# Kernel optimization log

Measured on AMD Instinct MI355X. Metric: run time of the kernel, lower is better.

Reference implementation:

```python
import jax, jax.numpy as jnp
import numpy as np

B, W, L = 32768, 5, 20            # batch, words per example, max chars per word
WV, CV = 50000, 100               # word vocab, char vocab
CE, OC, K = 32, 30, 3             # char embed dim, conv out channels (=window_size), kernel
WE, HID, TAGS = 50, 100, 36       # word embed dim, fc1 hidden, output tags


def setup_inputs() -> dict:
    key = jax.random.key(0)
    ks = jax.random.split(key, 8)
    inp = jax.random.randint(ks[0], (B, W, 1 + L), 0, 100, dtype=jnp.int32)
    embedding_matrix = jax.random.normal(ks[1], (WV, WE), jnp.float32).at[0].set(0.0)  # padding_idx=0, frozen
    char_emb = jax.random.normal(ks[2], (CV, CE), jnp.float32).at[0].set(0.0)          # padding_idx=0
    conv_w = jax.random.normal(ks[3], (OC, CE, K), jnp.float32) * 0.1
    conv_b = jnp.zeros((OC,), jnp.float32)
    fc1_w = jax.random.normal(ks[4], (HID, (WE + OC) * W), jnp.float32) * 0.05
    fc1_b = jnp.zeros((HID,), jnp.float32)
    out_w = jax.random.normal(ks[5], (TAGS, HID), jnp.float32) * 0.1
    out_b = jnp.zeros((TAGS,), jnp.float32)
    return dict(input=inp, embedding_matrix=embedding_matrix, char_emb=char_emb,
                conv_w=conv_w, conv_b=conv_b, fc1_w=fc1_w, fc1_b=fc1_b,
                out_w=out_w, out_b=out_b)


def reference(input, embedding_matrix, char_emb, conv_w, conv_b, fc1_w, fc1_b, out_w, out_b):
    b = input.shape[0]
    word_ids = input[:, :, 0]                 # [B, W]
    char_ids = input[:, :, 1:]                # [B, W, L]
    we = embedding_matrix[word_ids]           # [B, W, 50]
    ce = char_emb[char_ids]                   # [B, W, L, CE]
    # conv1d over char axis, batched over all B*W words at once
    x = ce.reshape(b * W, L, CE).transpose(0, 2, 1)        # [B*W, CE, L]
    conv = jax.lax.conv_general_dilated(
        x, conv_w, window_strides=(1,), padding='VALID',
        dimension_numbers=('NCH', 'OIH', 'NCH')) + conv_b[None, :, None]  # [B*W, OC, L-2]
    pooled = conv.max(axis=2).reshape(b, W, OC)            # max pool over time
    feats = jnp.concatenate([we, pooled], axis=-1).reshape(b, -1)  # [B, (50+OC)*W]
    h = jnp.tanh(feats @ fc1_w.T + fc1_b)     # dropout is a no-op at inference
    return h @ out_w.T + out_b                # [B, 36]
```

## Files before the change

kernel.cpp:

```cpp
#include <hip/hip_runtime.h>

#define B_TOT 32768
#define OC 30
#define HID 100
#define TAGS 36

#define WS_TH  0
#define WS_FC1 6000
#define WS_OUT 32624

typedef __attribute__((ext_vector_type(8))) _Float16 half8;
typedef __attribute__((ext_vector_type(2))) _Float16 h2v;
typedef __attribute__((ext_vector_type(4))) float f32x4;

__device__ inline half8 ash8(uint4 u) {
    union { uint4 a; half8 b; } v; v.a = u; return v.b;
}
__device__ inline unsigned int h2u(h2v h) {
    union { h2v a; unsigned int b; } v; v.a = h; return v.b;
}
__device__ inline h2v u2h(unsigned int u) {
    union { unsigned int a; h2v b; } v; v.a = u; return v.b;
}
__device__ inline unsigned int pk_f16(float a, float b) {
    h2v h; h.x = (_Float16)a; h.y = (_Float16)b; return h2u(h);
}
__device__ inline float fast_tanh(float x) {
    float ax = __builtin_fabsf(x);
    float e  = __expf(2.0f * ax);
    float r  = 1.0f - 2.0f * __builtin_amdgcn_rcpf(e + 1.0f);
    return __builtin_copysignf(r, x);
}

__global__ void prep(const float* __restrict__ conv_w,
                     const float* __restrict__ char_emb,
                     const float* __restrict__ fc1_w,
                     const float* __restrict__ out_w,
                     unsigned int* __restrict__ ws) {
    int idx = blockIdx.x * 256 + threadIdx.x;
    if (idx < 6000) {
        int d  = idx & 3;
        int t  = idx >> 2;
        int c  = t % 100;
        int kg = t / 100;
        int g  = kg % 5, k = kg / 5;
        int rd = g * 4 + d;
        float v[2];
        #pragma unroll
        for (int e = 0; e < 2; ++e) {
            int oc = rd * 2 + e;
            float s = 0.f;
            if (oc < OC) {
                for (int ce = 0; ce < 32; ++ce)
                    s += char_emb[c * 32 + ce] * conv_w[(oc * 32 + ce) * 3 + k];
            }
            v[e] = s;
        }
        ws[WS_TH + idx] = pk_f16(v[0], v[1]);
    } else if (idx < 6000 + 23296) {
        int t = idx - 6000;
        int dw = t & 3, lane = (t >> 2) & 63, chunk = t >> 8;
        int ks = chunk / 7, nt = chunk % 7;
        int j = nt * 16 + (lane & 15);
        int k = ks * 32 + (lane >> 4) * 8 + dw * 2;
        float a = (j < HID && k     < 400) ? fc1_w[j * 400 + k]     : 0.f;
        float b = (j < HID && k + 1 < 400) ? fc1_w[j * 400 + k + 1] : 0.f;
        ws[WS_FC1 + ks * 2048 + (nt * 64 + lane) * 4 + dw] = pk_f16(a, b);
    } else if (idx < 29296 + 3072) {
        int t = idx - 29296;
        int dw = t & 3, lane = (t >> 2) & 63, chunk = t >> 8;
        int ks = chunk / 3, nt = chunk % 3;
        int j = nt * 16 + (lane & 15);
        int k = ks * 32 + (lane >> 4) * 8 + dw * 2;
        float a = (j < TAGS && k     < HID) ? out_w[j * 100 + k]     : 0.f;
        float b = (j < TAGS && k + 1 < HID) ? out_w[j * 100 + k + 1] : 0.f;
        ws[WS_OUT + t] = pk_f16(a, b);
    }
}

__global__ __launch_bounds__(256, 2)
void fused(const int*   __restrict__ input,
           const float* __restrict__ emb,
           const float* __restrict__ conv_b,
           const float* __restrict__ fc1_b,
           const float* __restrict__ out_b,
           const unsigned int* __restrict__ ws,
           float*       __restrict__ out)
{
    __shared__ __align__(16) unsigned int Ths[6000];
    __shared__ __align__(16) unsigned int FL[64 * 212];

    const int tid  = threadIdx.x;
    const int wv   = tid >> 6;
    const int lane = tid & 63;
    const int ln15 = lane & 15;
    const int quad = lane >> 4;
    const int gi0  = blockIdx.x * 64 + wv * 16;
    unsigned int* Fw = &FL[wv * (16 * 212)];

    const uint4* srcB = (const uint4*)(ws + WS_FC1);
    const int se = wv * 128 + lane;

    {
        const uint4* src = (const uint4*)(ws + WS_TH);
        uint4* dst = (uint4*)Ths;
        for (int idx = tid; idx < 1500; idx += 256) dst[idx] = src[idx];
    }
    uint4 p0 = srcB[se], p1 = srcB[se + 64];
    __syncthreads();

    #pragma unroll
    for (int r = 0; r < 2; ++r) {
        int idx = lane + r * 64;
        Fw[(idx >> 3) * 212 + 200 + (idx & 7)] = 0;
    }

    #pragma unroll 4
    for (int idx = lane; idx < 2000; idx += 64) {
        int ph = idx % 25;
        int w  = (idx / 25) % 5;
        int i  = idx / 125;
        int wid = input[(gi0 + i) * 105 + w * 21];
        float2 e = *(const float2*)&emb[wid * 50 + ph * 2];
        Fw[i * 212 + w * 40 + ph] = pk_f16(e.x, e.y);
    }

    {
        const int q4  = lane & 3;
        const int oc0 = q4 * 8;
        h2v bias[4];
        #pragma unroll
        for (int d = 0; d < 4; ++d) {
            int a = oc0 + 2 * d, b = a + 1;
            bias[d].x = (_Float16)(a < OC ? conv_b[a] : 0.f);
            bias[d].y = (_Float16)(b < OC ? conv_b[b] : 0.f);
        }
        const unsigned int* T0 = &Ths[q4 * 400];
        const unsigned int* T1 = &Ths[q4 * 400 + 2000];
        const unsigned int* T2 = &Ths[q4 * 400 + 4000];
        #pragma unroll
        for (int it = 0; it < 5; ++it) {
            int task = (lane >> 2) + it * 16;
            int i = task / 5, w = task % 5;
            const int* cp = &input[(gi0 + i) * 105 + w * 21 + 1];
            int c[20];
            #pragma unroll
            for (int p = 0; p < 20; ++p) c[p] = cp[p];
            h2v m[4];
            #pragma unroll
            for (int d = 0; d < 4; ++d) { m[d].x = (_Float16)(-30000.f); m[d].y = (_Float16)(-30000.f); }
            #pragma unroll 6
            for (int p = 0; p < 18; ++p) {
                uint4 ra = *(const uint4*)&T0[c[p    ] * 4];
                uint4 rb = *(const uint4*)&T1[c[p + 1] * 4];
                uint4 rc = *(const uint4*)&T2[c[p + 2] * 4];
                unsigned int* pa = (unsigned int*)&ra;
                unsigned int* pb = (unsigned int*)&rb;
                unsigned int* pc = (unsigned int*)&rc;
                #pragma unroll
                for (int d = 0; d < 4; ++d) {
                    h2v s = u2h(pa[d]) + u2h(pb[d]) + u2h(pc[d]);
                    m[d] = __builtin_elementwise_max(m[d], s);
                }
            }
            int base = i * 212 + w * 40 + 25 + q4 * 4;
            Fw[base]     = h2u(m[0] + bias[0]);
            Fw[base + 1] = h2u(m[1] + bias[1]);
            Fw[base + 2] = h2u(m[2] + bias[2]);
            if (q4 < 3) Fw[base + 3] = h2u(m[3] + bias[3]);
        }
    }

    uint4 af[13];
    {
        const unsigned int* arow = &Fw[ln15 * 212 + quad * 4];
        #pragma unroll
        for (int ks = 0; ks < 13; ++ks) af[ks] = *(const uint4*)(arow + ks * 16);
    }

    f32x4 acc[7];
    #pragma unroll
    for (int t = 0; t < 7; ++t) acc[t] = f32x4{0, 0, 0, 0};

    uint4* Bb = (uint4*)Ths;
    __syncthreads();
    Bb[se] = p0; Bb[se + 64] = p1;
    __syncthreads();

    #pragma unroll
    for (int ks = 0; ks < 13; ++ks) {
        uint4 n0, n1;
        if (ks < 12) {
            n0 = srcB[(ks + 1) * 512 + se];
            n1 = srcB[(ks + 1) * 512 + se + 64];
        }
        const uint4* bp = Bb + (ks & 1) * 512;
        half8 a = ash8(af[ks]);
        #pragma unroll
        for (int t = 0; t < 7; ++t)
            acc[t] = __builtin_amdgcn_mfma_f32_16x16x32_f16(a, ash8(bp[t * 64 + lane]), acc[t], 0, 0, 0);
        if (ks < 12) {
            uint4* np = Bb + ((ks + 1) & 1) * 512;
            np[se] = n0; np[se + 64] = n1;
        }
        __syncthreads();
    }

    const uint4* srcO = (const uint4*)(ws + WS_OUT);
    uint4 o0 = srcO[wv * 192 + lane];
    uint4 o1 = srcO[wv * 192 + 64 + lane];
    uint4 o2 = srcO[wv * 192 + 128 + lane];

    unsigned int* Hw = Fw;
    {
        for (int t2 = lane; t2 < 224; t2 += 64) {
            int i = t2 / 14, d = t2 % 14;
            Hw[i * 68 + 50 + d] = 0;
        }
        unsigned short* Hs = (unsigned short*)Hw;
        #pragma unroll
        for (int t = 0; t < 7; ++t) {
            int j = t * 16 + ln15;
            if (j < HID) {
                float bj = fc1_b[j];
                #pragma unroll
                for (int r = 0; r < 4; ++r) {
                    int it = quad * 4 + r;
                    float hv = fast_tanh(acc[t][r] + bj);
                    _Float16 h = (_Float16)hv;
                    Hs[it * 136 + j] = *reinterpret_cast<unsigned short*>(&h);
                }
            }
        }
    }

    Bb[wv * 192 + lane]       = o0;
    Bb[wv * 192 + 64 + lane]  = o1;
    Bb[wv * 192 + 128 + lane] = o2;
    __syncthreads();

    {
        f32x4 oacc[3];
        #pragma unroll
        for (int t = 0; t < 3; ++t) oacc[t] = f32x4{0, 0, 0, 0};
        const int aoff = ln15 * 68 + quad * 4;
        #pragma unroll
        for (int ks = 0; ks < 4; ++ks) {
            half8 a = ash8(*(const uint4*)&Hw[aoff + ks * 16]);
            #pragma unroll
            for (int t = 0; t < 3; ++t) {
                uint4 bv = Bb[(ks * 3 + t) * 64 + lane];
                oacc[t] = __builtin_amdgcn_mfma_f32_16x16x32_f16(a, ash8(bv), oacc[t], 0, 0, 0);
            }
        }
        #pragma unroll
        for (int t = 0; t < 3; ++t) {
            int o = t * 16 + ln15;
            if (o < TAGS) {
                float bo = out_b[o];
                #pragma unroll
                for (int r = 0; r < 4; ++r) {
                    int it = gi0 + quad * 4 + r;
                    out[it * TAGS + o] = oacc[t][r] + bo;
                }
            }
        }
    }
}

extern "C" void kernel_launch(void* const* d_in, const int* in_sizes, int n_in,
                              void* d_out, int out_size, void* d_ws, size_t ws_size,
                              hipStream_t stream) {
    const int*   input  = (const int*)  d_in[0];
    const float* emb    = (const float*)d_in[1];
    const float* char_e = (const float*)d_in[2];
    const float* conv_w = (const float*)d_in[3];
    const float* conv_b = (const float*)d_in[4];
    const float* fc1_w  = (const float*)d_in[5];
    const float* fc1_b  = (const float*)d_in[6];
    const float* out_w  = (const float*)d_in[7];
    const float* out_b  = (const float*)d_in[8];
    unsigned int* ws = (unsigned int*)d_ws;

    prep<<<127, 256, 0, stream>>>(conv_w, char_e, fc1_w, out_w, ws);
    fused<<<B_TOT / 64, 256, 0, stream>>>(input, emb, conv_b, fc1_b, out_b, ws, (float*)d_out);
}
```

Baseline: 111.1 us.

## Triple-buffer fc1 weight staging and pad conv table rows against bank conflicts

The fc1 B-operand staging goes from a double buffer of 512 uint4 per k-step to a triple buffer of 448 uint4. Only the 7 real n-tiles are copied, with all 256 threads sharing the copy, and the global prefetch runs two steps ahead. One barrier is removed from the last iteration. The conv lookup table is re-laid out with each 400-word slice padded to 404 words, to spread LDS bank accesses across the four q4 groups, and the workspace offsets are realigned to match. This adds register pressure from holding extra prefetched vectors and makes the index math more fragile.

Measured after the change: 113.7 us. 1.02x slower.

```diff
diff --git a/kernel.cpp b/kernel.cpp
--- a/kernel.cpp
+++ b/kernel.cpp
@@ -6,8 +6,8 @@
 #define TAGS 36
 
 #define WS_TH  0
-#define WS_FC1 6000
-#define WS_OUT 32624
+#define WS_FC1 6144
+#define WS_OUT 32768
 
 typedef __attribute__((ext_vector_type(8))) _Float16 half8;
 typedef __attribute__((ext_vector_type(2))) _Float16 h2v;
@@ -43,8 +43,9 @@
         int t  = idx >> 2;
         int c  = t % 100;
         int kg = t / 100;
-        int g  = kg % 5, k = kg / 5;
+        int g  = kg % 5;
         int rd = g * 4 + d;
+        int k  = kg / 5;
         float v[2];
         #pragma unroll
         for (int e = 0; e < 2; ++e) {
@@ -56,7 +57,7 @@
             }
             v[e] = s;
         }
-        ws[WS_TH + idx] = pk_f16(v[0], v[1]);
+        ws[WS_TH + kg * 404 + c * 4 + d] = pk_f16(v[0], v[1]);
     } else if (idx < 6000 + 23296) {
         int t = idx - 6000;
         int dw = t & 3, lane = (t >> 2) & 63, chunk = t >> 8;
@@ -87,7 +88,7 @@
            const unsigned int* __restrict__ ws,
            float*       __restrict__ out)
 {
-    __shared__ __align__(16) unsigned int Ths[6000];
+    __shared__ __align__(16) unsigned int Ths[6060];
     __shared__ __align__(16) unsigned int FL[64 * 212];
 
     const int tid  = threadIdx.x;
@@ -96,17 +97,20 @@
     const int ln15 = lane & 15;
     const int quad = lane >> 4;
     const int gi0  = blockIdx.x * 64 + wv * 16;
+    const bool lo192 = (tid < 192);
     unsigned int* Fw = &FL[wv * (16 * 212)];
 
     const uint4* srcB = (const uint4*)(ws + WS_FC1);
-    const int se = wv * 128 + lane;
 
     {
         const uint4* src = (const uint4*)(ws + WS_TH);
         uint4* dst = (uint4*)Ths;
-        for (int idx = tid; idx < 1500; idx += 256) dst[idx] = src[idx];
-    }
-    uint4 p0 = srcB[se], p1 = srcB[se + 64];
+        for (int idx = tid; idx < 1515; idx += 256) dst[idx] = src[idx];
+    }
+    uint4 z4 = {0, 0, 0, 0};
+    uint4 pA0 = srcB[tid],        pA1 = lo192 ? srcB[256 + tid]        : z4;
+    uint4 pB0 = srcB[512 + tid],  pB1 = lo192 ? srcB[512 + 256 + tid]  : z4;
+    uint4 pC0 = srcB[1024 + tid], pC1 = lo192 ? srcB[1024 + 256 + tid] : z4;
     __syncthreads();
 
     #pragma unroll
@@ -135,9 +139,9 @@
             bias[d].x = (_Float16)(a < OC ? conv_b[a] : 0.f);
             bias[d].y = (_Float16)(b < OC ? conv_b[b] : 0.f);
         }
-        const unsigned int* T0 = &Ths[q4 * 400];
-        const unsigned int* T1 = &Ths[q4 * 400 + 2000];
-        const unsigned int* T2 = &Ths[q4 * 400 + 4000];
+        const unsigned int* T0 = &Ths[q4 * 404];
+        const unsigned int* T1 = &Ths[q4 * 404 + 2020];
+        const unsigned int* T2 = &Ths[q4 * 404 + 4040];
         #pragma unroll
         for (int it = 0; it < 5; ++it) {
             int task = (lane >> 2) + it * 16;
@@ -184,26 +188,30 @@
 
     uint4* Bb = (uint4*)Ths;
     __syncthreads();
-    Bb[se] = p0; Bb[se + 64] = p1;
-    __syncthreads();
+    Bb[tid] = pA0;            if (lo192) Bb[256 + tid] = pA1;
+    Bb[448 + tid] = pB0;      if (lo192) Bb[448 + 256 + tid] = pB1;
+    __syncthreads();
+    uint4 f0 = pC0, f1 = pC1;
 
     #pragma unroll
     for (int ks = 0; ks < 13; ++ks) {
-        uint4 n0, n1;
-        if (ks < 12) {
-            n0 = srcB[(ks + 1) * 512 + se];
-            n1 = srcB[(ks + 1) * 512 + se + 64];
-        }
-        const uint4* bp = Bb + (ks & 1) * 512;
+        uint4 n0 = z4, n1 = z4;
+        if (ks <= 9) {
+            n0 = srcB[(ks + 3) * 512 + tid];
+            if (lo192) n1 = srcB[(ks + 3) * 512 + 256 + tid];
+        }
+        const uint4* bp = Bb + (ks % 3) * 448;
         half8 a = ash8(af[ks]);
         #pragma unroll
         for (int t = 0; t < 7; ++t)
             acc[t] = __builtin_amdgcn_mfma_f32_16x16x32_f16(a, ash8(bp[t * 64 + lane]), acc[t], 0, 0, 0);
-        if (ks < 12) {
-            uint4* np = Bb + ((ks + 1) & 1) * 512;
-            np[se] = n0; np[se + 64] = n1;
-        }
-        __syncthreads();
+        if (ks <= 10) {
+            uint4* np = Bb + ((ks + 2) % 3) * 448;
+            np[tid] = f0;
+            if (lo192) np[256 + tid] = f1;
+        }
+        f0 = n0; f1 = n1;
+        if (ks <= 10 || ks == 12) __syncthreads();
     }
 
     const uint4* srcO = (const uint4*)(ws + WS_OUT);
```

## Precompute pairwise char-bigram conv table to replace two lookups per tap

Applied to the files above, without the earlier changes.

The first two conv taps are folded into a 100x100 bigram table computed in the prep kernel and read from global memory, leaving only the third tap in LDS. Each position now needs two gathers and one add instead of three gathers and two adds, and LDS use drops. The cost is a much larger prep kernel (160k extra threads, each doing a 32-element dot product) and random 640 KB global/L2 gathers in the main loop in place of cheap LDS reads.

New measurement: 132.6 us. 19.4% more time.

```diff
diff --git a/kernel.cpp b/kernel.cpp
--- a/kernel.cpp
+++ b/kernel.cpp
@@ -6,8 +6,9 @@
 #define TAGS 36
 
 #define WS_TH  0
-#define WS_FC1 6000
-#define WS_OUT 32624
+#define WS_TB  2048
+#define WS_FC1 162048
+#define WS_OUT 188672
 
 typedef __attribute__((ext_vector_type(8))) _Float16 half8;
 typedef __attribute__((ext_vector_type(2))) _Float16 h2v;
@@ -38,27 +39,41 @@
                      const float* __restrict__ out_w,
                      unsigned int* __restrict__ ws) {
     int idx = blockIdx.x * 256 + threadIdx.x;
-    if (idx < 6000) {
-        int d  = idx & 3;
-        int t  = idx >> 2;
-        int c  = t % 100;
-        int kg = t / 100;
-        int g  = kg % 5, k = kg / 5;
-        int rd = g * 4 + d;
+    if (idx < 1600) {
+        int d = idx & 15, c = idx >> 4;
         float v[2];
         #pragma unroll
         for (int e = 0; e < 2; ++e) {
-            int oc = rd * 2 + e;
+            int oc = 2 * d + e;
             float s = 0.f;
             if (oc < OC) {
                 for (int ce = 0; ce < 32; ++ce)
-                    s += char_emb[c * 32 + ce] * conv_w[(oc * 32 + ce) * 3 + k];
+                    s += char_emb[c * 32 + ce] * conv_w[(oc * 32 + ce) * 3 + 2];
             }
             v[e] = s;
         }
-        ws[WS_TH + idx] = pk_f16(v[0], v[1]);
-    } else if (idx < 6000 + 23296) {
-        int t = idx - 6000;
+        ws[WS_TH + c * 20 + d] = pk_f16(v[0], v[1]);
+    } else if (idx < 1600 + 160000) {
+        int t = idx - 1600;
+        int d = t & 15;
+        int pair = t >> 4;
+        int c1 = pair % 100, c0 = pair / 100;
+        float v[2];
+        #pragma unroll
+        for (int e = 0; e < 2; ++e) {
+            int oc = 2 * d + e;
+            float s = 0.f;
+            if (oc < OC) {
+                for (int ce = 0; ce < 32; ++ce) {
+                    s += char_emb[c0 * 32 + ce] * conv_w[(oc * 32 + ce) * 3 + 0]
+                       + char_emb[c1 * 32 + ce] * conv_w[(oc * 32 + ce) * 3 + 1];
+                }
+            }
+            v[e] = s;
+        }
+        ws[WS_TB + pair * 16 + d] = pk_f16(v[0], v[1]);
+    } else if (idx < 161600 + 23296) {
+        int t = idx - 161600;
         int dw = t & 3, lane = (t >> 2) & 63, chunk = t >> 8;
         int ks = chunk / 7, nt = chunk % 7;
         int j = nt * 16 + (lane & 15);
@@ -66,8 +81,8 @@
         float a = (j < HID && k     < 400) ? fc1_w[j * 400 + k]     : 0.f;
         float b = (j < HID && k + 1 < 400) ? fc1_w[j * 400 + k + 1] : 0.f;
         ws[WS_FC1 + ks * 2048 + (nt * 64 + lane) * 4 + dw] = pk_f16(a, b);
-    } else if (idx < 29296 + 3072) {
-        int t = idx - 29296;
+    } else if (idx < 184896 + 3072) {
+        int t = idx - 184896;
         int dw = t & 3, lane = (t >> 2) & 63, chunk = t >> 8;
         int ks = chunk / 3, nt = chunk % 3;
         int j = nt * 16 + (lane & 15);
@@ -87,7 +102,7 @@
            const unsigned int* __restrict__ ws,
            float*       __restrict__ out)
 {
-    __shared__ __align__(16) unsigned int Ths[6000];
+    __shared__ __align__(16) unsigned int Ths[4096];
     __shared__ __align__(16) unsigned int FL[64 * 212];
 
     const int tid  = threadIdx.x;
@@ -104,7 +119,7 @@
     {
         const uint4* src = (const uint4*)(ws + WS_TH);
         uint4* dst = (uint4*)Ths;
-        for (int idx = tid; idx < 1500; idx += 256) dst[idx] = src[idx];
+        for (int idx = tid; idx < 500; idx += 256) dst[idx] = src[idx];
     }
     uint4 p0 = srcB[se], p1 = srcB[se + 64];
     __syncthreads();
@@ -135,9 +150,8 @@
             bias[d].x = (_Float16)(a < OC ? conv_b[a] : 0.f);
             bias[d].y = (_Float16)(b < OC ? conv_b[b] : 0.f);
         }
-        const unsigned int* T0 = &Ths[q4 * 400];
-        const unsigned int* T1 = &Ths[q4 * 400 + 2000];
-        const unsigned int* T2 = &Ths[q4 * 400 + 4000];
+        const uint4* TBg = (const uint4*)(ws + WS_TB);
+        const unsigned int* T2 = Ths;
         #pragma unroll
         for (int it = 0; it < 5; ++it) {
             int task = (lane >> 2) + it * 16;
@@ -149,17 +163,15 @@
             h2v m[4];
             #pragma unroll
             for (int d = 0; d < 4; ++d) { m[d].x = (_Float16)(-30000.f); m[d].y = (_Float16)(-30000.f); }
-            #pragma unroll 6
+            #pragma unroll 9
             for (int p = 0; p < 18; ++p) {
-                uint4 ra = *(const uint4*)&T0[c[p    ] * 4];
-                uint4 rb = *(const uint4*)&T1[c[p + 1] * 4];
-                uint4 rc = *(const uint4*)&T2[c[p + 2] * 4];
-                unsigned int* pa = (unsigned int*)&ra;
-                unsigned int* pb = (unsigned int*)&rb;
-                unsigned int* pc = (unsigned int*)&rc;
+                uint4 rab = TBg[(c[p] * 100 + c[p + 1]) * 4 + q4];
+                uint4 rc  = *(const uint4*)&T2[c[p + 2] * 20 + q4 * 4];
+                unsigned int* pab = (unsigned int*)&rab;
+                unsigned int* pc  = (unsigned int*)&rc;
                 #pragma unroll
                 for (int d = 0; d < 4; ++d) {
-                    h2v s = u2h(pa[d]) + u2h(pb[d]) + u2h(pc[d]);
+                    h2v s = u2h(pab[d]) + u2h(pc[d]);
                     m[d] = __builtin_elementwise_max(m[d], s);
                 }
             }
@@ -282,6 +294,6 @@
     const float* out_b  = (const float*)d_in[8];
     unsigned int* ws = (unsigned int*)d_ws;
 
-    prep<<<127, 256, 0, stream>>>(conv_w, char_e, fc1_w, out_w, ws);
+    prep<<<735, 256, 0, stream>>>(conv_w, char_e, fc1_w, out_w, ws);
     fused<<<B_TOT / 64, 256, 0, stream>>>(input, emb, conv_b, fc1_b, out_b, ws, (float*)d_out);
 }
```

## Fold weight prep kernel into fused kernel, computing char-conv table per block via MFMA

Applied to the files above, without the earlier changes.

Removes the separate prep launch. Each block now builds the char_emb x conv_w lookup table in shared memory with MFMA, and converts fc1 and out weights from fp32 to fp16 on the fly while loading them. This drops one kernel launch and the workspace round trip. In exchange, all 512 blocks redo the table computation and read fp32 weights, which doubles the weight bytes loaded from L2.

New measurement: 119.5 us. 1.07x slower.

```diff
diff --git a/kernel.cpp b/kernel.cpp
--- a/kernel.cpp
+++ b/kernel.cpp
@@ -5,10 +5,6 @@
 #define HID 100
 #define TAGS 36
 
-#define WS_TH  0
-#define WS_FC1 6000
-#define WS_OUT 32624
-
 typedef __attribute__((ext_vector_type(8))) _Float16 half8;
 typedef __attribute__((ext_vector_type(2))) _Float16 h2v;
 typedef __attribute__((ext_vector_type(4))) float f32x4;
@@ -24,6 +20,14 @@
 }
 __device__ inline unsigned int pk_f16(float a, float b) {
     h2v h; h.x = (_Float16)a; h.y = (_Float16)b; return h2u(h);
+}
+__device__ inline uint4 pack8(float4 x, float4 y) {
+    uint4 r;
+    r.x = pk_f16(x.x, x.y);
+    r.y = pk_f16(x.z, x.w);
+    r.z = pk_f16(y.x, y.y);
+    r.w = pk_f16(y.z, y.w);
+    return r;
 }
 __device__ inline float fast_tanh(float x) {
     float ax = __builtin_fabsf(x);
@@ -32,59 +36,16 @@
     return __builtin_copysignf(r, x);
 }
 
-__global__ void prep(const float* __restrict__ conv_w,
-                     const float* __restrict__ char_emb,
-                     const float* __restrict__ fc1_w,
-                     const float* __restrict__ out_w,
-                     unsigned int* __restrict__ ws) {
-    int idx = blockIdx.x * 256 + threadIdx.x;
-    if (idx < 6000) {
-        int d  = idx & 3;
-        int t  = idx >> 2;
-        int c  = t % 100;
-        int kg = t / 100;
-        int g  = kg % 5, k = kg / 5;
-        int rd = g * 4 + d;
-        float v[2];
-        #pragma unroll
-        for (int e = 0; e < 2; ++e) {
-            int oc = rd * 2 + e;
-            float s = 0.f;
-            if (oc < OC) {
-                for (int ce = 0; ce < 32; ++ce)
-                    s += char_emb[c * 32 + ce] * conv_w[(oc * 32 + ce) * 3 + k];
-            }
-            v[e] = s;
-        }
-        ws[WS_TH + idx] = pk_f16(v[0], v[1]);
-    } else if (idx < 6000 + 23296) {
-        int t = idx - 6000;
-        int dw = t & 3, lane = (t >> 2) & 63, chunk = t >> 8;
-        int ks = chunk / 7, nt = chunk % 7;
-        int j = nt * 16 + (lane & 15);
-        int k = ks * 32 + (lane >> 4) * 8 + dw * 2;
-        float a = (j < HID && k     < 400) ? fc1_w[j * 400 + k]     : 0.f;
-        float b = (j < HID && k + 1 < 400) ? fc1_w[j * 400 + k + 1] : 0.f;
-        ws[WS_FC1 + ks * 2048 + (nt * 64 + lane) * 4 + dw] = pk_f16(a, b);
-    } else if (idx < 29296 + 3072) {
-        int t = idx - 29296;
-        int dw = t & 3, lane = (t >> 2) & 63, chunk = t >> 8;
-        int ks = chunk / 3, nt = chunk % 3;
-        int j = nt * 16 + (lane & 15);
-        int k = ks * 32 + (lane >> 4) * 8 + dw * 2;
-        float a = (j < TAGS && k     < HID) ? out_w[j * 100 + k]     : 0.f;
-        float b = (j < TAGS && k + 1 < HID) ? out_w[j * 100 + k + 1] : 0.f;
-        ws[WS_OUT + t] = pk_f16(a, b);
-    }
-}
-
 __global__ __launch_bounds__(256, 2)
 void fused(const int*   __restrict__ input,
            const float* __restrict__ emb,
+           const float* __restrict__ char_emb,
+           const float* __restrict__ conv_w,
            const float* __restrict__ conv_b,
+           const float* __restrict__ fc1_w,
            const float* __restrict__ fc1_b,
+           const float* __restrict__ out_w,
            const float* __restrict__ out_b,
-           const unsigned int* __restrict__ ws,
            float*       __restrict__ out)
 {
     __shared__ __align__(16) unsigned int Ths[6000];
@@ -98,16 +59,71 @@
     const int gi0  = blockIdx.x * 64 + wv * 16;
     unsigned int* Fw = &FL[wv * (16 * 212)];
 
-    const uint4* srcB = (const uint4*)(ws + WS_FC1);
     const int se = wv * 128 + lane;
-
-    {
-        const uint4* src = (const uint4*)(ws + WS_TH);
-        uint4* dst = (uint4*)Ths;
-        for (int idx = tid; idx < 1500; idx += 256) dst[idx] = src[idx];
-    }
-    uint4 p0 = srcB[se], p1 = srcB[se + 64];
+    const int jA = (2 * wv) * 16 + ln15;
+    const int jB = jA + 16;
+    const int kq = quad * 8;
+    const bool vA = (jA < HID), vB = (jB < HID);
+
+    float4 pa0{}, pa1{}, pb0{}, pb1{};
+    if (vA) { pa0 = *(const float4*)&fc1_w[jA * 400 + kq]; pa1 = *(const float4*)&fc1_w[jA * 400 + kq + 4]; }
+    if (vB) { pb0 = *(const float4*)&fc1_w[jB * 400 + kq]; pb1 = *(const float4*)&fc1_w[jB * 400 + kq + 4]; }
+
+    if (wv < 3) {
+        const int kk = wv;
+        half8 bfr[2];
+        #pragma unroll
+        for (int nt = 0; nt < 2; ++nt) {
+            int oc = nt * 16 + ln15;
+            union { h2v h[4]; half8 v; } u;
+            #pragma unroll
+            for (int d = 0; d < 4; ++d) {
+                int ce = kq + d * 2;
+                float a0 = (oc < OC) ? conv_w[(oc * 32 + ce) * 3 + kk]     : 0.f;
+                float a1 = (oc < OC) ? conv_w[(oc * 32 + ce + 1) * 3 + kk] : 0.f;
+                u.h[d].x = (_Float16)a0;
+                u.h[d].y = (_Float16)a1;
+            }
+            bfr[nt] = u.v;
+        }
+        unsigned short* Tu = (unsigned short*)Ths;
+        #pragma unroll
+        for (int mt = 0; mt < 7; ++mt) {
+            int c = mt * 16 + ln15;
+            float4 e0 = {0,0,0,0}, e1 = {0,0,0,0};
+            if (c < 100) {
+                e0 = *(const float4*)&char_emb[c * 32 + kq];
+                e1 = *(const float4*)&char_emb[c * 32 + kq + 4];
+            }
+            union { h2v h[4]; half8 v; } ua;
+            ua.h[0].x = (_Float16)e0.x; ua.h[0].y = (_Float16)e0.y;
+            ua.h[1].x = (_Float16)e0.z; ua.h[1].y = (_Float16)e0.w;
+            ua.h[2].x = (_Float16)e1.x; ua.h[2].y = (_Float16)e1.y;
+            ua.h[3].x = (_Float16)e1.z; ua.h[3].y = (_Float16)e1.w;
+            #pragma unroll
+            for (int nt = 0; nt < 2; ++nt) {
+                f32x4 tc = f32x4{0, 0, 0, 0};
+                tc = __builtin_amdgcn_mfma_f32_16x16x32_f16(ua.v, bfr[nt], tc, 0, 0, 0);
+                int oc = nt * 16 + ln15;
+                if (oc < OC) {
+                    int g = oc >> 3, dd = (oc >> 1) & 3, e = oc & 1;
+                    int ubase = kk * 4000 + g * 800 + dd * 2 + e;
+                    #pragma unroll
+                    for (int r = 0; r < 4; ++r) {
+                        int cc = mt * 16 + quad * 4 + r;
+                        if (cc < 100) {
+                            union { _Float16 f; unsigned short s; } cvt;
+                            cvt.f = (_Float16)tc[r];
+                            Tu[ubase + cc * 8] = cvt.s;
+                        }
+                    }
+                }
+            }
+        }
+    }
     __syncthreads();
+
+    uint4 p0 = pack8(pa0, pa1), p1 = pack8(pb0, pb1);
 
     #pragma unroll
     for (int r = 0; r < 2; ++r) {
@@ -189,10 +205,12 @@
 
     #pragma unroll
     for (int ks = 0; ks < 13; ++ks) {
-        uint4 n0, n1;
+        float4 na0{}, na1{}, nb0{}, nb1{};
         if (ks < 12) {
-            n0 = srcB[(ks + 1) * 512 + se];
-            n1 = srcB[(ks + 1) * 512 + se + 64];
+            const int kb = (ks + 1) * 32 + kq;
+            const bool kv = (ks < 11) || (kq <= 8);
+            if (vA && kv) { na0 = *(const float4*)&fc1_w[jA * 400 + kb]; na1 = *(const float4*)&fc1_w[jA * 400 + kb + 4]; }
+            if (vB && kv) { nb0 = *(const float4*)&fc1_w[jB * 400 + kb]; nb1 = *(const float4*)&fc1_w[jB * 400 + kb + 4]; }
         }
         const uint4* bp = Bb + (ks & 1) * 512;
         half8 a = ash8(af[ks]);
@@ -201,15 +219,29 @@
             acc[t] = __builtin_amdgcn_mfma_f32_16x16x32_f16(a, ash8(bp[t * 64 + lane]), acc[t], 0, 0, 0);
         if (ks < 12) {
             uint4* np = Bb + ((ks + 1) & 1) * 512;
-            np[se] = n0; np[se + 64] = n1;
+            np[se]      = pack8(na0, na1);
+            np[se + 64] = pack8(nb0, nb1);
         }
         __syncthreads();
     }
 
-    const uint4* srcO = (const uint4*)(ws + WS_OUT);
-    uint4 o0 = srcO[wv * 192 + lane];
-    uint4 o1 = srcO[wv * 192 + 64 + lane];
-    uint4 o2 = srcO[wv * 192 + 128 + lane];
+    uint4 og[3];
+    {
+        const int ko = wv * 32 + kq;
+        #pragma unroll
+        for (int nt = 0; nt < 3; ++nt) {
+            int j = nt * 16 + ln15;
+            unsigned int dws[4];
+            #pragma unroll
+            for (int dw = 0; dw < 4; ++dw) {
+                int kk = ko + dw * 2;
+                float a = (j < TAGS && kk     < HID) ? out_w[j * 100 + kk]     : 0.f;
+                float b = (j < TAGS && kk + 1 < HID) ? out_w[j * 100 + kk + 1] : 0.f;
+                dws[dw] = pk_f16(a, b);
+            }
+            og[nt].x = dws[0]; og[nt].y = dws[1]; og[nt].z = dws[2]; og[nt].w = dws[3];
+        }
+    }
 
     unsigned int* Hw = Fw;
     {
@@ -234,9 +266,9 @@
         }
     }
 
-    Bb[wv * 192 + lane]       = o0;
-    Bb[wv * 192 + 64 + lane]  = o1;
-    Bb[wv * 192 + 128 + lane] = o2;
+    Bb[wv * 192 + lane]       = og[0];
+    Bb[wv * 192 + 64 + lane]  = og[1];
+    Bb[wv * 192 + 128 + lane] = og[2];
     __syncthreads();
 
     {
@@ -280,8 +312,7 @@
     const float* fc1_b  = (const float*)d_in[6];
     const float* out_w  = (const float*)d_in[7];
     const float* out_b  = (const float*)d_in[8];
-    unsigned int* ws = (unsigned int*)d_ws;
-
-    prep<<<127, 256, 0, stream>>>(conv_w, char_e, fc1_w, out_w, ws);
-    fused<<<B_TOT / 64, 256, 0, stream>>>(input, emb, conv_b, fc1_b, out_b, ws, (float*)d_out);
-}
+
+    fused<<<B_TOT / 64, 256, 0, stream>>>(input, emb, char_e, conv_w, conv_b,
+                                          fc1_w, fc1_b, out_w, out_b, (float*)d_out);
+}
```
